# Optimization experiments

Hardware: AMD Instinct MI355X
Metric: run time of the kernel (lower is better)

Reference implementation:

```python
import jax, jax.numpy as jnp
import numpy as np

B, Lq, D = 2, 4096, 768
NH, NP, NL = 6, 4, 1
Hs, Ws = 128, 128
Lf = Hs * Ws
DH = D // NH
EPS = 1e-6


def _ln(x, g, b):
    m = jnp.mean(x, -1, keepdims=True)
    v = jnp.mean(jnp.square(x - m), -1, keepdims=True)
    return (x - m) * jax.lax.rsqrt(v + EPS) * g + b


def setup_inputs() -> dict:
    key = jax.random.key(0)
    ks = jax.random.split(key, 20)
    s = 0.02
    rn = lambda k, shape, sc=s: (jax.random.normal(k, shape, jnp.float32) * sc)
    return {
        'query': jax.random.normal(ks[0], (B, Lq, D), jnp.float32),
        'reference_points': jax.random.uniform(ks[1], (B, Lq, NL, 2), jnp.float32),
        'feat': jax.random.normal(ks[2], (B, Lf, D), jnp.float32),
        'feat_other_modalities': jax.random.normal(ks[3], (B, Lq, D), jnp.float32),
        'spatial_shapes': jnp.array([[Hs, Ws]], jnp.int32),
        'level_start_index': jnp.array([0], jnp.int32),
        'qn_g': jnp.ones(D), 'qn_b': jnp.zeros(D),
        'fn_g': jnp.ones(D), 'fn_b': jnp.zeros(D),
        'W_off': rn(ks[4], (D, NH * NL * NP * 2)), 'b_off': jnp.zeros(NH * NL * NP * 2),
        'W_attn': rn(ks[5], (D, NH * NL * NP)), 'b_attn': jnp.zeros(NH * NL * NP),
        'W_val': rn(ks[6], (D, D)), 'b_val': jnp.zeros(D),
        'W_out': rn(ks[7], (D, D)), 'b_out': jnp.zeros(D),
        'gamma': rn(ks[8], (D,), 0.1),
        'qnm_g': jnp.ones(D), 'qnm_b': jnp.zeros(D),
        'fnm_g': jnp.ones(D), 'fnm_b': jnp.zeros(D),
        'ada_w0': rn(ks[9], (D, D // 4)), 'ada_b0': jnp.zeros(D // 4),
        'ada_w1': rn(ks[10], (D, D // 4)), 'ada_b1': jnp.zeros(D // 4),
        'ada_w2': rn(ks[11], (D // 4, D)), 'ada_b2': jnp.zeros(D),
        'gamma_om': rn(ks[12], (D,), 0.1),
    }


def _msdeform_attn(query_n, reference_points, feat_n, Hi, Wi,
                   W_off, b_off, W_attn, b_attn, W_val, b_val, W_out, b_out):
    Bv = query_n.shape[0]
    value = (feat_n @ W_val + b_val).reshape(Bv, Lf, NH, DH)
    value = value.transpose(0, 2, 1, 3)  # (B, NH, Lf, DH)

    off = (query_n @ W_off + b_off).reshape(Bv, Lq, NH, NL, NP, 2)
    aw = (query_n @ W_attn + b_attn).reshape(Bv, Lq, NH, NL * NP)
    aw = jax.nn.softmax(aw, axis=-1).reshape(Bv, Lq, NH, NL, NP)

    normalizer = jnp.array([Wi, Hi], jnp.float32)  # [W, H]
    loc = reference_points[:, :, None, :, None, :] + off / normalizer  # (B,Lq,NH,NL,NP,2)
    loc = loc[:, :, :, 0]  # single level -> (B, Lq, NH, NP, 2)

    # grid_sample align_corners=False, padding zeros
    x = loc[..., 0] * Wi - 0.5
    y = loc[..., 1] * Hi - 0.5
    x0 = jnp.floor(x); y0 = jnp.floor(y)
    wx1 = x - x0; wx0 = 1.0 - wx1
    wy1 = y - y0; wy0 = 1.0 - wy1
    x0i = x0.astype(jnp.int32); y0i = y0.astype(jnp.int32)
    x1i = x0i + 1; y1i = y0i + 1

    def t(a):  # (B,Lq,NH,NP) -> (B,NH,Lq,NP,1)
        return a.transpose(0, 2, 1, 3)[..., None]

    def gather(yy, xx):
        valid = (xx >= 0) & (xx < Wi) & (yy >= 0) & (yy < Hi)
        idx = jnp.clip(yy, 0, Hi - 1) * Wi + jnp.clip(xx, 0, Wi - 1)  # (B,Lq,NH,NP)
        idx = idx.transpose(0, 2, 1, 3).reshape(Bv, NH, Lq * NP)
        g = jnp.take_along_axis(value, idx[..., None], axis=2)  # (B,NH,Lq*NP,DH)
        g = g.reshape(Bv, NH, Lq, NP, DH)
        return g * t(valid.astype(jnp.float32))

    sampled = (gather(y0i, x0i) * t(wy0 * wx0) + gather(y0i, x1i) * t(wy0 * wx1)
               + gather(y1i, x0i) * t(wy1 * wx0) + gather(y1i, x1i) * t(wy1 * wx1))
    awT = aw[:, :, :, 0].transpose(0, 2, 1, 3)[..., None]  # (B,NH,Lq,NP,1)
    out = jnp.sum(sampled * awT, axis=3)  # (B,NH,Lq,DH)
    out = out.transpose(0, 2, 1, 3).reshape(Bv, Lq, D)
    return out @ W_out + b_out


def reference(query, reference_points, feat, feat_other_modalities, spatial_shapes,
              level_start_index, qn_g, qn_b, fn_g, fn_b, W_off, b_off, W_attn, b_attn,
              W_val, b_val, W_out, b_out, gamma, qnm_g, qnm_b, fnm_g, fnm_b,
              ada_w0, ada_b0, ada_w1, ada_b1, ada_w2, ada_b2, gamma_om):
    Hi = int(np.asarray(spatial_shapes)[0, 0]); Wi = int(np.asarray(spatial_shapes)[0, 1])
    query_n = _ln(query, qn_g, qn_b)
    feat_n = _ln(feat, fn_g, fn_b)
    attn = _msdeform_attn(query_n, reference_points, feat_n, Hi, Wi,
                          W_off, b_off, W_attn, b_attn, W_val, b_val, W_out, b_out)
    q = query + gamma * attn
    fom_n = _ln(feat_other_modalities, fnm_g, fnm_b)
    qn2 = _ln(q, qnm_g, qnm_b)
    p = qn2 @ ada_w0 + ada_b0
    xm = fom_n @ ada_w1 + ada_b1
    prompted = (p + xm) @ ada_w2 + ada_b2
    q = q + gamma_om * prompted
    return (q, prompted)
```

## Files before the change

### kernel.cpp

```cpp
#include <hip/hip_runtime.h>
#include <hip/hip_bf16.h>

typedef long long i64;

#define B_   2
#define LQ   4096
#define D_   768
#define NH_  6
#define NP_  4
#define DH_  128
#define LF   16384
#define NQ_ROWS (B_*LQ)
#define NF_ROWS (B_*LF)
#define QSIZE (NQ_ROWS*D_)
#define R_TOT (NF_ROWS + 2*NQ_ROWS)
#define LN_BLOCKS (R_TOT/8)

typedef __bf16 bf16x8 __attribute__((ext_vector_type(8)));
typedef float  f32x4  __attribute__((ext_vector_type(4)));

__device__ __forceinline__ int probe_bf(const void* probe) {
  return (*(const unsigned*)probe == 0x3F803F80u) ? 1 : 0;
}
__device__ __forceinline__ float load_in(const void* p, i64 i, int bf) {
  if (bf) return __bfloat162float(((const __hip_bfloat16*)p)[i]);
  return ((const float*)p)[i];
}
__device__ __forceinline__ float us2f(unsigned short u) {
  unsigned v = (unsigned)u << 16;
  return __uint_as_float(v);
}
__device__ __forceinline__ unsigned short f2us(float f) {
  __hip_bfloat16 h = __float2bfloat16(f);
  return *(unsigned short*)&h;
}

#define NCVT 17
struct CvtArgs { const void* src[NCVT]; const void* src2[NCVT]; float* dst[NCVT]; int n[NCVT]; const void* probe; };
__global__ void k_cvt(CvtArgs a) {
  int bf = probe_bf(a.probe);
  int ai = blockIdx.y;
  int n = a.n[ai];
  const void* s = a.src[ai];
  const void* s2 = a.src2[ai];
  float* d = a.dst[ai];
  for (int i = blockIdx.x * blockDim.x + threadIdx.x; i < n; i += gridDim.x * blockDim.x) {
    float v = load_in(s, i, bf);
    if (s2) v += load_in(s2, i, bf);
    d[i] = v;
  }
}

__device__ __forceinline__ void ln_load_bf16(const void* src, i64 so, int sl, uint4* u) {
  const unsigned short* s = (const unsigned short*)src + so;
  #pragma unroll
  for (int j = 0; j < 3; ++j) u[j] = *(const uint4*)(s + (i64)(j * 32 + sl) * 8);
}
__device__ __forceinline__ void ln_load_f32(const void* src, i64 so, int sl, float4* w) {
  const float* s = (const float*)src + so;
  #pragma unroll
  for (int j = 0; j < 3; ++j) {
    w[2*j]   = *(const float4*)(s + (i64)(j * 32 + sl) * 8);
    w[2*j+1] = *(const float4*)(s + (i64)(j * 32 + sl) * 8 + 4);
  }
}
__device__ __forceinline__ void ln_unpack_bf16(const uint4* u, float* v) {
  #pragma unroll
  for (int j = 0; j < 3; ++j) {
    uint4 t = u[j];
    v[j*8+0] = us2f((unsigned short)t.x); v[j*8+1] = us2f((unsigned short)(t.x >> 16));
    v[j*8+2] = us2f((unsigned short)t.y); v[j*8+3] = us2f((unsigned short)(t.y >> 16));
    v[j*8+4] = us2f((unsigned short)t.z); v[j*8+5] = us2f((unsigned short)(t.z >> 16));
    v[j*8+6] = us2f((unsigned short)t.w); v[j*8+7] = us2f((unsigned short)(t.w >> 16));
  }
}
__device__ __forceinline__ void ln_unpack_f32(const float4* w, float* v) {
  #pragma unroll
  for (int j = 0; j < 6; ++j) {
    v[j*4+0] = w[j].x; v[j*4+1] = w[j].y; v[j*4+2] = w[j].z; v[j*4+3] = w[j].w;
  }
}
__device__ __forceinline__ void ln_finish(const float* v, const float* g, const float* b,
                                          unsigned short* dp, int sl) {
  float s1 = 0.f, s2 = 0.f;
  #pragma unroll
  for (int i = 0; i < 24; ++i) { s1 += v[i]; s2 += v[i] * v[i]; }
  #pragma unroll
  for (int o = 16; o > 0; o >>= 1) { s1 += __shfl_xor(s1, o, 64); s2 += __shfl_xor(s2, o, 64); }
  float mean = s1 * (1.f / 768.f);
  float var  = s2 * (1.f / 768.f) - mean * mean;
  float rstd = rsqrtf(var + 1e-6f);
  #pragma unroll
  for (int j = 0; j < 3; ++j) {
    int gi = (j * 32 + sl) * 8;
    float4 g0 = *(const float4*)(g + gi), g1 = *(const float4*)(g + gi + 4);
    float4 b0 = *(const float4*)(b + gi), b1 = *(const float4*)(b + gi + 4);
    uint4 o;
    o.x = (unsigned)f2us((v[j*8+0]-mean)*rstd*g0.x+b0.x) | ((unsigned)f2us((v[j*8+1]-mean)*rstd*g0.y+b0.y) << 16);
    o.y = (unsigned)f2us((v[j*8+2]-mean)*rstd*g0.z+b0.z) | ((unsigned)f2us((v[j*8+3]-mean)*rstd*g0.w+b0.w) << 16);
    o.z = (unsigned)f2us((v[j*8+4]-mean)*rstd*g1.x+b1.x) | ((unsigned)f2us((v[j*8+5]-mean)*rstd*g1.y+b1.y) << 16);
    o.w = (unsigned)f2us((v[j*8+6]-mean)*rstd*g1.z+b1.z) | ((unsigned)f2us((v[j*8+7]-mean)*rstd*g1.w+b1.w) << 16);
    *(uint4*)(dp + gi) = o;
  }
}

#define NTT 7
struct StageArgs {
  const void* tsrc[NTT]; __hip_bfloat16* tdst[NTT];
  int K[NTT]; int N[NTT]; int Nt[NTT]; int ds[NTT];
  int tileBase[NTT]; int tilesN[NTT];
  const void* feat; const void* query; const void* fom;
  const float *fg, *fb, *qg, *qb, *mg, *mb;
  __hip_bfloat16 *featn, *qn, *qnf;
  void* qraw;
  const void* probe;
};
__global__ void k_stage(StageArgs a) {
  __shared__ float lds[64][65];
  int bf = probe_bf(a.probe);
  if ((int)blockIdx.x >= LN_BLOCKS) {
    int t = blockIdx.x - LN_BLOCKS;
    int e = 0;
    #pragma unroll
    for (int i = 1; i < NTT; ++i) if (t >= a.tileBase[i]) e = i;
    int lt = t - a.tileBase[e];
    int tn = lt % a.tilesN[e], tk = lt / a.tilesN[e];
    int K = a.K[e], N = a.N[e], Nt = a.Nt[e], ds = a.ds[e];
    int k0 = tk * 64, n0 = tn * 64;
    int tid = threadIdx.x;
    int cl = tid & 63, rw = tid >> 6;
    const void* s = a.tsrc[e];
    #pragma unroll
    for (int i = 0; i < 16; ++i) {
      int kl = rw * 16 + i;
      int n = n0 + cl;
      float v = (n < N) ? load_in(s, (i64)(k0 + kl) * N + n, bf) : 0.f;
      lds[kl][cl] = v;
    }
    __syncthreads();
    __hip_bfloat16* d = a.tdst[e];
    #pragma unroll
    for (int i = 0; i < 16; ++i) {
      int nl = rw * 16 + i;
      int n = n0 + nl;
      if (n < Nt) d[(i64)n * ds + k0 + cl] = __float2bfloat16(lds[cl][nl]);
    }
    return;
  }
  int row = blockIdx.x * 8 + (threadIdx.x >> 5);
  int sl = threadIdx.x & 31;
  const void* s; const float *g, *b; unsigned short* dp; i64 so; int kind; int lr;
  if (row < NF_ROWS) {
    kind = 0; lr = row; s = a.feat; so = (i64)lr * 768;
    g = a.fg; b = a.fb; dp = (unsigned short*)a.featn + (i64)lr * 768;
  } else if (row < NF_ROWS + NQ_ROWS) {
    kind = 1; lr = row - NF_ROWS; s = a.query; so = (i64)lr * 768;
    g = a.qg; b = a.qb; dp = (unsigned short*)a.qn + (i64)lr * 768;
  } else {
    kind = 2; lr = row - NF_ROWS - NQ_ROWS; s = a.fom; so = (i64)lr * 768;
    g = a.mg; b = a.mb; dp = (unsigned short*)a.qnf + (i64)lr * 1536 + 768;
  }
  float v[24];
  if (bf) {
    uint4 u[3];
    ln_load_bf16(s, so, sl, u);
    if (kind == 1) {
      unsigned short* qr = (unsigned short*)a.qraw + (i64)lr * 768;
      #pragma unroll
      for (int j = 0; j < 3; ++j) *(uint4*)(qr + (i64)(j * 32 + sl) * 8) = u[j];
    }
    ln_unpack_bf16(u, v);
  } else {
    float4 w[6];
    ln_load_f32(s, so, sl, w);
    if (kind == 1) {
      float* qr = (float*)a.qraw + (i64)lr * 768;
      #pragma unroll
      for (int j = 0; j < 3; ++j) {
        *(float4*)(qr + (i64)(j * 32 + sl) * 8)     = w[2*j];
        *(float4*)(qr + (i64)(j * 32 + sl) * 8 + 4) = w[2*j+1];
      }
    }
    ln_unpack_f32(w, v);
  }
  ln_finish(v, g, b, dp, sl);
}

__global__ void k_ln_q(const float* src, const float* g, const float* b, __hip_bfloat16* dst) {
  int hw = blockIdx.x * 8 + (threadIdx.x >> 5);
  int sl = threadIdx.x & 31;
  int r = hw * 2;
  float4 w0[6], w1[6];
  ln_load_f32(src, (i64)r * 768, sl, w0);
  ln_load_f32(src, (i64)(r + 1) * 768, sl, w1);
  float v[24];
  ln_unpack_f32(w0, v);
  ln_finish(v, g, b, (unsigned short*)dst + (i64)r * 1536, sl);
  ln_unpack_f32(w1, v);
  ln_finish(v, g, b, (unsigned short*)dst + (i64)(r + 1) * 1536, sl);
}

__device__ __forceinline__ void load_lds16(const void* g, void* l) {
  __builtin_amdgcn_global_load_lds((__attribute__((address_space(1))) void*)g,
                                   (__attribute__((address_space(3))) void*)l, 16, 0, 0);
}

template<int EPI>
__global__ void k_mgemm(const __hip_bfloat16* __restrict__ A, const __hip_bfloat16* __restrict__ Wt,
                        const float* __restrict__ bias, void* __restrict__ Cp,
                        int M, int N, int K, int Nx,
                        const void* aux0, const float* __restrict__ aux1, const void* probe) {
  __shared__ __align__(16) __hip_bfloat16 sm[2 * 8192];
  __hip_bfloat16* As = sm;
  __hip_bfloat16* Bs = sm + 8192;
  const int tid  = threadIdx.x;
  const int w    = tid >> 6, lane = tid & 63;
  const int quad = lane >> 4, l15 = lane & 15;
  const int f = blockIdx.x;
  const int xcd = f & 7, s8 = f >> 3;
  const int bn = (s8 % Nx) * 128;
  const int bm = (xcd + (s8 / Nx) * 8) * 128;
  const int wm = (w >> 1) * 64, wn = (w & 1) * 64;
  const int bfv = (EPI == 2 || EPI == 3) ? probe_bf(probe) : 0;

  int rowS[4], colS[4];
  #pragma unroll
  for (int j = 0; j < 4; ++j) {
    int p = j * 256 + tid;
    int r = p >> 3, pc = p & 7;
    rowS[j] = r; colS[j] = (pc ^ (r & 7)) * 8;
  }

  f32x4 acc[4][4];
  #pragma unroll
  for (int i = 0; i < 4; ++i)
    #pragma unroll
    for (int j = 0; j < 4; ++j) acc[i][j] = (f32x4){0.f, 0.f, 0.f, 0.f};

  const __hip_bfloat16* Ab = A  + (i64)bm * K;
  const __hip_bfloat16* Bb = Wt + (i64)bn * K;

  for (int k0 = 0; k0 < K; k0 += 64) {
    #pragma unroll
    for (int j = 0; j < 4; ++j) {
      load_lds16(Ab + (i64)rowS[j] * K + k0 + colS[j], As + (j * 256 + w * 64) * 8);
      load_lds16(Bb + (i64)rowS[j] * K + k0 + colS[j], Bs + (j * 256 + w * 64) * 8);
    }
    __syncthreads();
    bf16x8 af[2][4], bg[2][4];
    #pragma unroll
    for (int s = 0; s < 2; ++s) {
      #pragma unroll
      for (int i = 0; i < 4; ++i) {
        int ra = wm + i * 16 + l15;
        af[s][i] = *(const bf16x8*)(As + (ra * 8 + ((s * 4 + quad) ^ (ra & 7))) * 8);
        int rb = wn + i * 16 + l15;
        bg[s][i] = *(const bf16x8*)(Bs + (rb * 8 + ((s * 4 + quad) ^ (rb & 7))) * 8);
      }
    }
    #pragma unroll
    for (int s = 0; s < 2; ++s)
      #pragma unroll
      for (int i = 0; i < 4; ++i)
        #pragma unroll
        for (int j = 0; j < 4; ++j)
          acc[i][j] = __builtin_amdgcn_mfma_f32_16x16x32_bf16(af[s][i], bg[s][j], acc[i][j], 0, 0, 0);
    __syncthreads();
  }

  #pragma unroll
  for (int j = 0; j < 4; ++j) {
    int col = bn + wn + j * 16 + l15;
    if (col >= N) continue;
    float bv = bias[col];
    #pragma unroll
    for (int i = 0; i < 4; ++i) {
      #pragma unroll
      for (int r = 0; r < 4; ++r) {
        int row = bm + wm + i * 16 + quad * 4 + r;
        float v = acc[i][j][r] + bv;
        i64 idx = (i64)row * N + col;
        if (EPI == 0) {
          ((__hip_bfloat16*)Cp)[idx] = __float2bfloat16(v);
        } else if (EPI == 1) {
          ((float*)Cp)[idx] = v;
        } else if (EPI == 2) {
          ((float*)Cp)[idx] = load_in(aux0, idx, bfv) + aux1[col] * v;
        } else {
          float qv = ((const float*)aux0)[idx] + aux1[col] * v;
          if (bfv) {
            ((__hip_bfloat16*)Cp)[idx]         = __float2bfloat16(qv);
            ((__hip_bfloat16*)Cp)[QSIZE + idx] = __float2bfloat16(v);
          } else {
            ((float*)Cp)[idx]         = qv;
            ((float*)Cp)[QSIZE + idx] = v;
          }
        }
      }
    }
  }
}

__global__ void k_sample(const __hip_bfloat16* __restrict__ val, const float* __restrict__ ref,
                         const float* __restrict__ oa, const int* __restrict__ ss,
                         __hip_bfloat16* __restrict__ out) {
  int gw = blockIdx.x * 4 + (threadIdx.x >> 6);
  if (gw >= NQ_ROWS) return;
  int lane = threadIdx.x & 63;
  int sg = lane >> 4, sl = lane & 15;
  int bq = gw, b = bq >> 12;
  int Hi = ss[0], Wi = ss[1];
  float Wf = (float)Wi, Hf = (float)Hi;
  float rx = ref[(i64)bq*2], ry = ref[(i64)bq*2 + 1];
  const float* orow = oa + (i64)bq * 72;
  const __hip_bfloat16* vb = val + (i64)b * LF * D_;
  int cx = sg & 1, cy = sg >> 1;
  #pragma unroll
  for (int h = 0; h < NH_; ++h) {
    const float* ap = orow + 48 + h*4;
    float a0 = ap[0], a1 = ap[1], a2 = ap[2], a3 = ap[3];
    float mx = fmaxf(fmaxf(a0, a1), fmaxf(a2, a3));
    float e0 = __expf(a0-mx), e1 = __expf(a1-mx), e2 = __expf(a2-mx), e3 = __expf(a3-mx);
    float inv = 1.0f / (e0+e1+e2+e3);
    float wts[4] = {e0*inv, e1*inv, e2*inv, e3*inv};
    const float* op = orow + h*8;
    float acc[8];
    #pragma unroll
    for (int e = 0; e < 8; ++e) acc[e] = 0.f;
    #pragma unroll
    for (int p = 0; p < NP_; ++p) {
      float x = rx*Wf + op[p*2+0] - 0.5f;
      float y = ry*Hf + op[p*2+1] - 0.5f;
      float xf = floorf(x), yf = floorf(y);
      int x0 = (int)xf, y0 = (int)yf;
      float wx1 = x - xf, wy1 = y - yf;
      int xi = x0 + cx, yi = y0 + cy;
      float wgt = wts[p] * (cx ? wx1 : 1.f - wx1) * (cy ? wy1 : 1.f - wy1);
      if (xi >= 0 && xi < Wi && yi >= 0 && yi < Hi) {
        bf16x8 g = *(const bf16x8*)(vb + (i64)(yi*Wi + xi)*D_ + h*DH_ + sl*8);
        #pragma unroll
        for (int e = 0; e < 8; ++e) acc[e] += wgt * (float)g[e];
      }
    }
    #pragma unroll
    for (int e = 0; e < 8; ++e) {
      acc[e] += __shfl_xor(acc[e], 16, 64);
      acc[e] += __shfl_xor(acc[e], 32, 64);
    }
    if (sg == 0) {
      uint4 o;
      o.x = (unsigned)f2us(acc[0]) | ((unsigned)f2us(acc[1]) << 16);
      o.y = (unsigned)f2us(acc[2]) | ((unsigned)f2us(acc[3]) << 16);
      o.z = (unsigned)f2us(acc[4]) | ((unsigned)f2us(acc[5]) << 16);
      o.w = (unsigned)f2us(acc[6]) | ((unsigned)f2us(acc[7]) << 16);
      *(uint4*)(out + (i64)bq*D_ + h*DH_ + sl*8) = o;
    }
  }
}

extern "C" void kernel_launch(void* const* d_in, const int* in_sizes, int n_in,
                              void* d_out, int out_size, void* d_ws, size_t ws_size,
                              hipStream_t stream) {
  char* base = (char*)d_ws;
  size_t o = 0;
  auto alloc = [&](size_t bytes) { size_t r = o; o += (bytes + 63) & ~(size_t)63; return r; };
  auto F = [&](size_t off) { return (float*)(base + off); };
  auto H = [&](size_t off) { return (__hip_bfloat16*)(base + off); };
  const void* probe = d_in[6];

  size_t REF   = alloc(NQ_ROWS*2*4);
  size_t QN_G  = alloc(768*4); size_t QN_B = alloc(768*4);
  size_t FN_G  = alloc(768*4); size_t FN_B = alloc(768*4);
  size_t BOA   = alloc(128*4);
  size_t BVAL  = alloc(768*4); size_t BOUT = alloc(768*4);
  size_t GAMMA = alloc(768*4);
  size_t QNM_G = alloc(768*4); size_t QNM_B = alloc(768*4);
  size_t FNM_G = alloc(768*4); size_t FNM_B = alloc(768*4);
  size_t AB01  = alloc(192*4);
  size_t AB2   = alloc(768*4); size_t GOM  = alloc(768*4);
  size_t WT_VAL = alloc((size_t)768*768*2);
  size_t WT_OUT = alloc((size_t)768*768*2);
  size_t WT_OA  = alloc((size_t)128*768*2);
  size_t WT_A01 = alloc((size_t)256*1536*2);
  size_t WT_A2  = alloc((size_t)768*192*2);
  size_t FEATN  = alloc((size_t)NF_ROWS*768*2);
  size_t VALUE  = alloc((size_t)NF_ROWS*768*2);
  size_t QN     = alloc((size_t)NQ_ROWS*768*2);
  size_t QRAW   = alloc((size_t)QSIZE*4);
  size_t QNF    = alloc((size_t)NQ_ROWS*1536*2);
  size_t ATTNP  = alloc((size_t)NQ_ROWS*768*2);
  size_t PXM    = alloc((size_t)NQ_ROWS*192*2);
  size_t OA     = alloc((size_t)NQ_ROWS*72*4);
  size_t QBUF   = alloc((size_t)QSIZE*4);

  {
    CvtArgs ca;
    const int   idx[NCVT]  = {1,6,7,8,9,11,13,15,17,18,19,20,21,22,24,28,29};
    const size_t dof[NCVT] = {REF,QN_G,QN_B,FN_G,FN_B,BOA,BOA+48*4,BVAL,BOUT,GAMMA,
                              QNM_G,QNM_B,FNM_G,FNM_B,AB01,AB2,GOM};
    for (int i = 0; i < NCVT; ++i) {
      ca.src[i] = d_in[idx[i]]; ca.src2[i] = nullptr;
      ca.dst[i] = F(dof[i]); ca.n[i] = in_sizes[idx[i]];
    }
    ca.src2[14] = d_in[26];
    ca.probe = probe;
    k_cvt<<<dim3(8, NCVT), 256, 0, stream>>>(ca);
  }

  int tb = 0;
  {
    StageArgs sa;
    const int   src[NTT]  = {14, 16, 10, 12, 23, 25, 27};
    const size_t dst[NTT] = {WT_VAL, WT_OUT, WT_OA, WT_OA + (size_t)48*768*2,
                             WT_A01, WT_A01 + (size_t)768*2, WT_A2};
    const int Kk[NTT] = {768, 768, 768, 768, 768,  768, 192};
    const int Nn[NTT] = {768, 768,  48,  24, 192,  192, 768};
    const int Nt[NTT] = {768, 768,  48,  80, 256,  256, 768};
    const int Ds[NTT] = {768, 768, 768, 768, 1536, 1536, 192};
    for (int i = 0; i < NTT; ++i) {
      sa.tsrc[i] = d_in[src[i]]; sa.tdst[i] = H(dst[i]);
      sa.K[i] = Kk[i]; sa.N[i] = Nn[i]; sa.Nt[i] = Nt[i]; sa.ds[i] = Ds[i];
      sa.tilesN[i] = (Nt[i] + 63) / 64;
      sa.tileBase[i] = tb;
      tb += sa.tilesN[i] * (Kk[i] / 64);
    }
    sa.feat = d_in[2]; sa.query = d_in[0]; sa.fom = d_in[3];
    sa.fg = F(FN_G);  sa.fb = F(FN_B);
    sa.qg = F(QN_G);  sa.qb = F(QN_B);
    sa.mg = F(FNM_G); sa.mb = F(FNM_B);
    sa.featn = H(FEATN); sa.qn = H(QN); sa.qnf = H(QNF);
    sa.qraw = base + QRAW;
    sa.probe = probe;
    k_stage<<<LN_BLOCKS + tb, 256, 0, stream>>>(sa);
  }

  k_mgemm<0><<<256*6, 256, 0, stream>>>(H(FEATN), H(WT_VAL), F(BVAL), H(VALUE),
                                        NF_ROWS, 768, 768, 6, nullptr, nullptr, probe);
  k_mgemm<1><<<64*1, 256, 0, stream>>>(H(QN), H(WT_OA), F(BOA), F(OA),
                                       NQ_ROWS, 72, 768, 1, nullptr, nullptr, probe);
  k_sample<<<NQ_ROWS/4, 256, 0, stream>>>(H(VALUE), F(REF), F(OA), (const int*)d_in[4], H(ATTNP));
  k_mgemm<2><<<64*6, 256, 0, stream>>>(H(ATTNP), H(WT_OUT), F(BOUT), F(QBUF),
                                       NQ_ROWS, 768, 768, 6, base + QRAW, F(GAMMA), probe);
  k_ln_q<<<NQ_ROWS/16, 256, 0, stream>>>(F(QBUF), F(QNM_G), F(QNM_B), H(QNF));
  k_mgemm<0><<<64*2, 256, 0, stream>>>(H(QNF), H(WT_A01), F(AB01), H(PXM),
                                       NQ_ROWS, 192, 1536, 2, nullptr, nullptr, probe);
  k_mgemm<3><<<64*6, 256, 0, stream>>>(H(PXM), H(WT_A2), F(AB2), d_out,
                                       NQ_ROWS, 768, 192, 6, F(QBUF), F(GOM), probe);
}
```

Baseline: 458.9 us.

## Fold feature LayerNorm into value GEMM via per-row stats and column sums

Removes the separate LayerNorm pass over the large feature tensor and its bf16 intermediate. The value GEMM now computes per-row mean and rstd itself and multiplies raw features by gamma-scaled weights, then applies rstd*acc - rstd*mean*colsum(gamma*W) + colsum(beta*W) + bias in the epilogue. This saves a full read and write of the normalized features. In exchange, each of the six column-tile blocks per row tile recomputes the row statistics, the fp32 input path converts to bf16 without async LDS loads, and the var = E[x^2] - mean^2 form is less accurate than the two-pass variance.

```diff
diff --git a/kernel.cpp b/kernel.cpp
--- a/kernel.cpp
+++ b/kernel.cpp
@@ -13,8 +13,7 @@
 #define NQ_ROWS (B_*LQ)
 #define NF_ROWS (B_*LF)
 #define QSIZE (NQ_ROWS*D_)
-#define R_TOT (NF_ROWS + 2*NQ_ROWS)
-#define LN_BLOCKS (R_TOT/8)
+#define LN2_BLOCKS (2*NQ_ROWS/8)
 
 typedef __bf16 bf16x8 __attribute__((ext_vector_type(8)));
 typedef float  f32x4  __attribute__((ext_vector_type(4)));
@@ -51,6 +50,29 @@
   }
 }
 
+__global__ void k_colsum(const void* w, const void* g, const void* b,
+                         float* c, float* d, const void* probe) {
+  __shared__ float red[2][4][64];
+  int bf = probe_bf(probe);
+  int l = threadIdx.x & 63;
+  int kc = threadIdx.x >> 6;
+  int j = blockIdx.x * 64 + l;
+  int k0 = kc * 192;
+  float cs = 0.f, ds = 0.f;
+  #pragma unroll 8
+  for (int k = 0; k < 192; ++k) {
+    float wv = load_in(w, (i64)(k0 + k) * 768 + j, bf);
+    cs += load_in(g, k0 + k, bf) * wv;
+    ds += load_in(b, k0 + k, bf) * wv;
+  }
+  red[0][kc][l] = cs; red[1][kc][l] = ds;
+  __syncthreads();
+  if (kc == 0) {
+    c[j] = red[0][0][l] + red[0][1][l] + red[0][2][l] + red[0][3][l];
+    d[j] = red[1][0][l] + red[1][1][l] + red[1][2][l] + red[1][3][l];
+  }
+}
+
 __device__ __forceinline__ void ln_load_bf16(const void* src, i64 so, int sl, uint4* u) {
   const unsigned short* s = (const unsigned short*)src + so;
   #pragma unroll
@@ -107,19 +129,20 @@
 #define NTT 7
 struct StageArgs {
   const void* tsrc[NTT]; __hip_bfloat16* tdst[NTT];
+  const void* tscale[NTT];
   int K[NTT]; int N[NTT]; int Nt[NTT]; int ds[NTT];
   int tileBase[NTT]; int tilesN[NTT];
-  const void* feat; const void* query; const void* fom;
-  const float *fg, *fb, *qg, *qb, *mg, *mb;
-  __hip_bfloat16 *featn, *qn, *qnf;
+  const void* query; const void* fom;
+  const float *qg, *qb, *mg, *mb;
+  __hip_bfloat16 *qn, *qnf;
   void* qraw;
   const void* probe;
 };
 __global__ void k_stage(StageArgs a) {
   __shared__ float lds[64][65];
   int bf = probe_bf(a.probe);
-  if ((int)blockIdx.x >= LN_BLOCKS) {
-    int t = blockIdx.x - LN_BLOCKS;
+  if ((int)blockIdx.x >= LN2_BLOCKS) {
+    int t = blockIdx.x - LN2_BLOCKS;
     int e = 0;
     #pragma unroll
     for (int i = 1; i < NTT; ++i) if (t >= a.tileBase[i]) e = i;
@@ -130,11 +153,13 @@
     int tid = threadIdx.x;
     int cl = tid & 63, rw = tid >> 6;
     const void* s = a.tsrc[e];
+    const void* sc = a.tscale[e];
     #pragma unroll
     for (int i = 0; i < 16; ++i) {
       int kl = rw * 16 + i;
       int n = n0 + cl;
       float v = (n < N) ? load_in(s, (i64)(k0 + kl) * N + n, bf) : 0.f;
+      if (sc) v *= load_in(sc, k0 + kl, bf);
       lds[kl][cl] = v;
     }
     __syncthreads();
@@ -150,14 +175,11 @@
   int row = blockIdx.x * 8 + (threadIdx.x >> 5);
   int sl = threadIdx.x & 31;
   const void* s; const float *g, *b; unsigned short* dp; i64 so; int kind; int lr;
-  if (row < NF_ROWS) {
-    kind = 0; lr = row; s = a.feat; so = (i64)lr * 768;
-    g = a.fg; b = a.fb; dp = (unsigned short*)a.featn + (i64)lr * 768;
-  } else if (row < NF_ROWS + NQ_ROWS) {
-    kind = 1; lr = row - NF_ROWS; s = a.query; so = (i64)lr * 768;
+  if (row < NQ_ROWS) {
+    kind = 1; lr = row; s = a.query; so = (i64)lr * 768;
     g = a.qg; b = a.qb; dp = (unsigned short*)a.qn + (i64)lr * 768;
   } else {
-    kind = 2; lr = row - NF_ROWS - NQ_ROWS; s = a.fom; so = (i64)lr * 768;
+    kind = 2; lr = row - NQ_ROWS; s = a.fom; so = (i64)lr * 768;
     g = a.mg; b = a.mb; dp = (unsigned short*)a.qnf + (i64)lr * 1536 + 768;
   }
   float v[24];
@@ -203,6 +225,126 @@
 __device__ __forceinline__ void load_lds16(const void* g, void* l) {
   __builtin_amdgcn_global_load_lds((__attribute__((address_space(1))) void*)g,
                                    (__attribute__((address_space(3))) void*)l, 16, 0, 0);
+}
+
+__global__ void k_vgemm(const void* __restrict__ Araw, const __hip_bfloat16* __restrict__ Wt,
+                        const float* __restrict__ bias, __hip_bfloat16* __restrict__ Cp,
+                        const float* __restrict__ cv, const float* __restrict__ dv,
+                        const void* probe) {
+  __shared__ __align__(16) __hip_bfloat16 sm[2 * 8192];
+  __shared__ float rowstat[128][2];
+  __hip_bfloat16* As = sm;
+  __hip_bfloat16* Bs = sm + 8192;
+  const int tid  = threadIdx.x;
+  const int w    = tid >> 6, lane = tid & 63;
+  const int quad = lane >> 4, l15 = lane & 15;
+  const int f = blockIdx.x;
+  const int xcd = f & 7, s8 = f >> 3;
+  const int bn = (s8 % 6) * 128;
+  const int bm = (xcd + (s8 / 6) * 8) * 128;
+  const int wm = (w >> 1) * 64, wn = (w & 1) * 64;
+  const int bfv = probe_bf(probe);
+
+  {
+    int sl = tid & 31, hw = tid >> 5;
+    #pragma unroll 2
+    for (int pass = 0; pass < 16; ++pass) {
+      int r = pass * 8 + hw;
+      float v[24];
+      if (bfv) { uint4 u[3]; ln_load_bf16(Araw, (i64)(bm + r) * 768, sl, u); ln_unpack_bf16(u, v); }
+      else     { float4 wv[6]; ln_load_f32(Araw, (i64)(bm + r) * 768, sl, wv); ln_unpack_f32(wv, v); }
+      float s1 = 0.f, s2 = 0.f;
+      #pragma unroll
+      for (int i = 0; i < 24; ++i) { s1 += v[i]; s2 += v[i] * v[i]; }
+      #pragma unroll
+      for (int o = 16; o > 0; o >>= 1) { s1 += __shfl_xor(s1, o, 64); s2 += __shfl_xor(s2, o, 64); }
+      if (sl == 0) {
+        float mean = s1 * (1.f / 768.f);
+        float var  = s2 * (1.f / 768.f) - mean * mean;
+        float rstd = rsqrtf(var + 1e-6f);
+        rowstat[r][0] = rstd; rowstat[r][1] = -rstd * mean;
+      }
+    }
+  }
+  __syncthreads();
+
+  int rowS[4], colS[4];
+  #pragma unroll
+  for (int j = 0; j < 4; ++j) {
+    int p = j * 256 + tid;
+    int r = p >> 3, pc = p & 7;
+    rowS[j] = r; colS[j] = (pc ^ (r & 7)) * 8;
+  }
+
+  f32x4 acc[4][4];
+  #pragma unroll
+  for (int i = 0; i < 4; ++i)
+    #pragma unroll
+    for (int j = 0; j < 4; ++j) acc[i][j] = (f32x4){0.f, 0.f, 0.f, 0.f};
+
+  const __hip_bfloat16* Ab = (const __hip_bfloat16*)Araw + (i64)bm * 768;
+  const __hip_bfloat16* Bb = Wt + (i64)bn * 768;
+
+  for (int k0 = 0; k0 < 768; k0 += 64) {
+    if (bfv) {
+      #pragma unroll
+      for (int j = 0; j < 4; ++j)
+        load_lds16(Ab + (i64)rowS[j] * 768 + k0 + colS[j], As + (j * 256 + w * 64) * 8);
+    } else {
+      #pragma unroll
+      for (int j = 0; j < 4; ++j) {
+        int p = j * 256 + tid;
+        int r = p >> 3, pc = p & 7;
+        const float* src = (const float*)Araw + (i64)(bm + r) * 768 + k0 + pc * 8;
+        float4 x0 = *(const float4*)src;
+        float4 x1 = *(const float4*)(src + 4);
+        uint4 o;
+        o.x = (unsigned)f2us(x0.x) | ((unsigned)f2us(x0.y) << 16);
+        o.y = (unsigned)f2us(x0.z) | ((unsigned)f2us(x0.w) << 16);
+        o.z = (unsigned)f2us(x1.x) | ((unsigned)f2us(x1.y) << 16);
+        o.w = (unsigned)f2us(x1.z) | ((unsigned)f2us(x1.w) << 16);
+        *(uint4*)(As + ((i64)r * 8 + (pc ^ (r & 7))) * 8) = o;
+      }
+    }
+    #pragma unroll
+    for (int j = 0; j < 4; ++j)
+      load_lds16(Bb + (i64)rowS[j] * 768 + k0 + colS[j], Bs + (j * 256 + w * 64) * 8);
+    __syncthreads();
+    bf16x8 af[2][4], bg[2][4];
+    #pragma unroll
+    for (int s = 0; s < 2; ++s) {
+      #pragma unroll
+      for (int i = 0; i < 4; ++i) {
+        int ra = wm + i * 16 + l15;
+        af[s][i] = *(const bf16x8*)(As + (ra * 8 + ((s * 4 + quad) ^ (ra & 7))) * 8);
+        int rb = wn + i * 16 + l15;
+        bg[s][i] = *(const bf16x8*)(Bs + (rb * 8 + ((s * 4 + quad) ^ (rb & 7))) * 8);
+      }
+    }
+    #pragma unroll
+    for (int s = 0; s < 2; ++s)
+      #pragma unroll
+      for (int i = 0; i < 4; ++i)
+        #pragma unroll
+        for (int j = 0; j < 4; ++j)
+          acc[i][j] = __builtin_amdgcn_mfma_f32_16x16x32_bf16(af[s][i], bg[s][j], acc[i][j], 0, 0, 0);
+    __syncthreads();
+  }
+
+  #pragma unroll
+  for (int j = 0; j < 4; ++j) {
+    int col = bn + wn + j * 16 + l15;
+    float cj = cv[col], dj = dv[col] + bias[col];
+    #pragma unroll
+    for (int i = 0; i < 4; ++i) {
+      #pragma unroll
+      for (int r = 0; r < 4; ++r) {
+        int lr = wm + i * 16 + quad * 4 + r;
+        float v = rowstat[lr][0] * acc[i][j][r] + rowstat[lr][1] * cj + dj;
+        Cp[(i64)(bm + lr) * 768 + col] = __float2bfloat16(v);
+      }
+    }
+  }
 }
 
 template<int EPI>
@@ -378,12 +520,12 @@
   size_t FNM_G = alloc(768*4); size_t FNM_B = alloc(768*4);
   size_t AB01  = alloc(192*4);
   size_t AB2   = alloc(768*4); size_t GOM  = alloc(768*4);
+  size_t CV    = alloc(768*4); size_t DV   = alloc(768*4);
   size_t WT_VAL = alloc((size_t)768*768*2);
   size_t WT_OUT = alloc((size_t)768*768*2);
   size_t WT_OA  = alloc((size_t)128*768*2);
   size_t WT_A01 = alloc((size_t)256*1536*2);
   size_t WT_A2  = alloc((size_t)768*192*2);
-  size_t FEATN  = alloc((size_t)NF_ROWS*768*2);
   size_t VALUE  = alloc((size_t)NF_ROWS*768*2);
   size_t QN     = alloc((size_t)NQ_ROWS*768*2);
   size_t QRAW   = alloc((size_t)QSIZE*4);
@@ -406,6 +548,7 @@
     ca.probe = probe;
     k_cvt<<<dim3(8, NCVT), 256, 0, stream>>>(ca);
   }
+  k_colsum<<<12, 256, 0, stream>>>(d_in[14], d_in[8], d_in[9], F(CV), F(DV), probe);
 
   int tb = 0;
   {
@@ -417,25 +560,25 @@
     const int Nn[NTT] = {768, 768,  48,  24, 192,  192, 768};
     const int Nt[NTT] = {768, 768,  48,  80, 256,  256, 768};
     const int Ds[NTT] = {768, 768, 768, 768, 1536, 1536, 192};
+    const void* sc[NTT] = {d_in[8], nullptr, nullptr, nullptr, nullptr, nullptr, nullptr};
     for (int i = 0; i < NTT; ++i) {
-      sa.tsrc[i] = d_in[src[i]]; sa.tdst[i] = H(dst[i]);
+      sa.tsrc[i] = d_in[src[i]]; sa.tdst[i] = H(dst[i]); sa.tscale[i] = sc[i];
       sa.K[i] = Kk[i]; sa.N[i] = Nn[i]; sa.Nt[i] = Nt[i]; sa.ds[i] = Ds[i];
       sa.tilesN[i] = (Nt[i] + 63) / 64;
       sa.tileBase[i] = tb;
       tb += sa.tilesN[i] * (Kk[i] / 64);
     }
-    sa.feat = d_in[2]; sa.query = d_in[0]; sa.fom = d_in[3];
-    sa.fg = F(FN_G);  sa.fb = F(FN_B);
+    sa.query = d_in[0]; sa.fom = d_in[3];
     sa.qg = F(QN_G);  sa.qb = F(QN_B);
     sa.mg = F(FNM_G); sa.mb = F(FNM_B);
-    sa.featn = H(FEATN); sa.qn = H(QN); sa.qnf = H(QNF);
+    sa.qn = H(QN); sa.qnf = H(QNF);
     sa.qraw = base + QRAW;
     sa.probe = probe;
-    k_stage<<<LN_BLOCKS + tb, 256, 0, stream>>>(sa);
-  }
-
-  k_mgemm<0><<<256*6, 256, 0, stream>>>(H(FEATN), H(WT_VAL), F(BVAL), H(VALUE),
-                                        NF_ROWS, 768, 768, 6, nullptr, nullptr, probe);
+    k_stage<<<LN2_BLOCKS + tb, 256, 0, stream>>>(sa);
+  }
+
+  k_vgemm<<<256*6, 256, 0, stream>>>(d_in[2], H(WT_VAL), F(BVAL), H(VALUE),
+                                     F(CV), F(DV), probe);
   k_mgemm<1><<<64*1, 256, 0, stream>>>(H(QN), H(WT_OA), F(BOA), F(OA),
                                        NQ_ROWS, 72, 768, 1, nullptr, nullptr, probe);
   k_sample<<<NQ_ROWS/4, 256, 0, stream>>>(H(VALUE), F(REF), F(OA), (const int*)d_in[4], H(ATTNP));
```

After: 565.6 us. 1.23x slower.
